# Optimization experiments

Measured on AMD Instinct MI355X. Metric: run time of the kernel, lower is better.

Reference implementation:

```python
import jax, jax.numpy as jnp
import numpy as np

HID = 1024            # hidden_dim
COND = 80             # cond_dim (mel bins)
EMB = HID // 8        # 128
D = HID // 4          # 256
NC = 2 ** 8           # num_coarse_bits = 8
NF = 2 ** 8           # num_fine_bits = 8
N, L = 32, 1024


def _vs(key, shape):
    # VarianceScaling(1.0, fan_in, truncated_normal) approximated by normal/sqrt(fan_in)
    return jax.random.normal(key, shape, jnp.float32) / jnp.sqrt(jnp.float32(shape[0]))


def setup_inputs() -> dict:
    key = jax.random.key(0)
    ks = jax.random.split(key, 16)
    x = jax.random.randint(ks[0], (N, L, 2), 0, NC, dtype=jnp.int64)
    mel = jax.random.normal(ks[1], (N, L, COND), jnp.float32)
    return {
        "x": x,
        "mel": mel,
        "R_w": _vs(ks[2], (HID, 3 * HID)),
        "R_b": jnp.zeros((3 * HID,), jnp.float32),
        "I_W": _vs(ks[3], (COND + 3 * EMB, 3 * HID)),
        "I_b": jnp.zeros((1, 3 * HID), jnp.float32),
        "O1_w": _vs(ks[4], (3 * D, 3 * D)),
        "O1_b": jnp.zeros((3 * D,), jnp.float32),
        "O2_w": _vs(ks[5], (3 * D, NC)),
        "O2_b": jnp.zeros((NC,), jnp.float32),
        "O3_w": _vs(ks[6], (D, D)),
        "O3_b": jnp.zeros((D,), jnp.float32),
        "O4_w": _vs(ks[7], (D, NF)),
        "O4_b": jnp.zeros((NF,), jnp.float32),
        "c_emb": jax.random.normal(ks[8], (NC, EMB), jnp.float32) * 0.02,
        "f_emb": jax.random.normal(ks[9], (NF, EMB), jnp.float32) * 0.02,
    }


def _mask_like(I_W):
    # zero out future-coarse embedding rows for the coarse-prediction gate halves
    m = jnp.ones_like(I_W)
    m = m.at[-EMB:, 0 * D:3 * D].set(0.0)
    m = m.at[-EMB:, 4 * D:7 * D].set(0.0)
    m = m.at[-EMB:, 8 * D:11 * D].set(0.0)
    return m


def _forward(x, mel, R_w, R_b, I_W, I_b, O1_w, O1_b, O2_w, O2_b, O3_w, O3_b, O4_w, O4_b, c_emb, f_emb):
    c = x[..., 0]
    f = x[..., 1]
    c_next = jnp.roll(c, -1, -1)
    # [N, L, COND + 3*EMB]
    inp = jnp.concatenate((mel, c_emb[c], f_emb[f], c_emb[c_next]), axis=-1)
    IW = I_W * _mask_like(I_W)
    # input projection is time-independent -> precompute for all steps: [N, L, 3H]
    xproj = jnp.einsum("nld,dh->nlh", inp, IW) + I_b[0]

    def step(h, xt):
        u1, r1, e1 = jnp.split(h @ R_w + R_b, 3, axis=-1)
        u2, r2, e2 = jnp.split(xt, 3, axis=-1)
        u = jax.nn.sigmoid(u1 + u2)
        r = jax.nn.sigmoid(r1 + r2)
        e = jnp.tanh(r * e1 + e2)
        h = u * h + (1.0 - u) * e
        return h, h

    h0 = jnp.zeros((x.shape[0], HID), xproj.dtype)
    _, hs = jax.lax.scan(step, h0, jnp.swapaxes(xproj, 0, 1))  # [L, N, H]
    hs = jnp.swapaxes(hs, 0, 1)                                 # [N, L, H]
    yc = hs[..., : 3 * D]
    yf = hs[..., 3 * D:]
    clogits = jax.nn.relu(yc @ O1_w + O1_b) @ O2_w + O2_b
    flogits = jax.nn.relu(yf @ O3_w + O3_b) @ O4_w + O4_b
    return clogits, flogits


def reference(x, mel, R_w, R_b, I_W, I_b, O1_w, O1_b, O2_w, O2_b, O3_w, O3_b, O4_w, O4_b, c_emb, f_emb):
    return _forward(x, mel, R_w, R_b, I_W, I_b, O1_w, O1_b, O2_w, O2_b,
                    O3_w, O3_b, O4_w, O4_b, c_emb, f_emb)
```

## Files before the change

kernel.cpp:

```cpp
#include <hip/hip_runtime.h>
#include <hip/hip_bf16.h>
#include <math.h>

typedef __attribute__((ext_vector_type(4))) float vf4;
typedef __attribute__((ext_vector_type(8))) short vbf8;
typedef __attribute__((ext_vector_type(8))) unsigned short vus8;

#define NWG   128
#define NTHR  256
#define LEN   1024
#define H3    3072
#define CND   80
#define EMBD  128

#define TAB1_B  0ull
#define TAB2_B  (TAB1_B + 786432ull*4)
#define TAB3_B  (TAB2_B + 786432ull*4)
#define BF_B    (TAB3_B + 786432ull*4)
#define MELA_B  (BF_B   + 4587520ull*2)
#define AF_B    (MELA_B + 3145728ull*2)
#define CNT_B   (AF_B   + 33587200ull*2)
#define W1F_B   (CNT_B + 4096ull)
#define W2F_B   (W1F_B + 1179648ull)
#define W3F_B   (W2F_B + 393216ull)
#define W4F_B   (W3F_B + 131072ull)
#define FOFS    8388608ull


__global__ __launch_bounds__(256) void make_tables(const float* __restrict__ IW,
                                                   const float* __restrict__ Ib,
                                                   const float* __restrict__ cemb,
                                                   const float* __restrict__ femb,
                                                   float* __restrict__ tab1,
                                                   float* __restrict__ tab2,
                                                   float* __restrict__ tab3) {
    int blk = blockIdx.x;
    int table = blk / 3072;
    int rem = blk % 3072;
    int row = rem / 12;
    int cc = rem % 12;
    int col = cc * 256 + threadIdx.x;
    int ofs = CND + table * EMBD;
    const float* emb = (table == 1) ? femb : cemb;
    float acc = 0.f;
    for (int k = 0; k < EMBD; ++k)
        acc += emb[row * EMBD + k] * IW[(size_t)(ofs + k) * H3 + col];
    if (table == 0) acc += Ib[col];
    if (table == 2 && ((col & 1023) < 768)) acc = 0.f;
    float* dst = (table == 0) ? tab1 : (table == 1 ? tab2 : tab3);
    dst[(size_t)row * H3 + col] = acc;
}

__global__ __launch_bounds__(256) void build_bfrag2(const float* __restrict__ Rw,
                                                    const float* __restrict__ IW,
                                                    const float* __restrict__ Rb,
                                                    unsigned short* __restrict__ Bf) {
    int idx = blockIdx.x * 256 + threadIdx.x;
    int col = idx % 3072;
    int k   = idx / 3072;
    float v;
    if (k < 1024)       v = Rw[(size_t)k * H3 + col];
    else if (k < 1104)  v = IW[(size_t)(k - 1024) * H3 + col];
    else if (k == 1104) v = Rb[col];
    else return;

    int g  = col >> 10;
    int j  = col & 1023;
    int oct = j >> 3, jo = j & 7;
    int which, c;
    if (g < 2)      { which = 0; c = g * 8 + jo; }
    else {
        which = 1;
        if (k < 1024 || k == 1104) c = jo;
        else                        c = 8 + jo;
    }
    int kk = k >> 5, r5 = k & 31;
    int lane = (r5 >> 3) * 16 + c;
    int elem = r5 & 7;
    size_t dst = (((size_t)oct * 2 + which) * 35 + kk) * 512 + lane * 8 + elem;
    __hip_bfloat16 hb = __float2bfloat16(v);
    Bf[dst] = *(unsigned short*)&hb;
}

__global__ __launch_bounds__(256) void build_melA(const float* __restrict__ mel,
                                                  unsigned short* __restrict__ MelA) {
    long idx = (long)blockIdx.x * 256 + threadIdx.x;
    int elem = idx & 7;
    int lane = (idx >> 3) & 63;
    int kkm  = (int)((idx >> 9) % 3);
    int m    = (int)((idx / 1536) & 1);
    int t    = (int)(idx / 3072);
    int b    = m * 16 + (lane & 15);
    int km   = kkm * 32 + ((lane >> 4) & 3) * 8 + elem;
    float v = (km < CND) ? mel[((size_t)b * LEN + t) * CND + km] : (km == CND ? 1.f : 0.f);
    __hip_bfloat16 hb = __float2bfloat16(v);
    MelA[idx] = *(unsigned short*)&hb;
}

__global__ __launch_bounds__(256) void build_wfrag(const float* __restrict__ W,
                                                   unsigned short* __restrict__ Wf,
                                                   int K, int N) {
    int idx = blockIdx.x * 256 + threadIdx.x;
    if (idx >= K * N) return;
    int col = idx % N;
    int k   = idx / N;
    int nt = col >> 4, c = col & 15;
    int kf = k >> 5, k5 = k & 31;
    int lane = c + 16 * (k5 >> 3);
    int elem = k5 & 7;
    size_t dst = ((size_t)nt * (K >> 5) + kf) * 512 + (size_t)lane * 8 + elem;
    __hip_bfloat16 hb = __float2bfloat16(W[idx]);
    Wf[dst] = *(unsigned short*)&hb;
}

__device__ __forceinline__ int is_sent(unsigned long long q) {
    return ((unsigned)q == 0xFFFFFFFFu) || ((unsigned)(q >> 32) == 0xFFFFFFFFu);
}

__global__ __launch_bounds__(256, 1) void scan_persist(const unsigned short* __restrict__ Bf,
                                                       const unsigned short* __restrict__ MelA,
                                                       unsigned short* __restrict__ Af,
                                                       const float* __restrict__ tab1,
                                                       const float* __restrict__ tab2,
                                                       const float* __restrict__ tab3,
                                                       const int* __restrict__ xin) {
    __shared__ float pex[4][4][256];

    int tid = threadIdx.x;
    int wg  = blockIdx.x;
    int lane = tid & 63;
    int wv = tid >> 6;
    int bh = wg >> 6;
    int jg = wg & 63;

    const unsigned short* Bp0 = Bf + (((size_t)(jg * 2 + 0) * 2 + 0) * 35) * 512 + lane * 8;
    const unsigned short* Bp1 = Bf + (((size_t)(jg * 2 + 0) * 2 + 1) * 35) * 512 + lane * 8;
    const unsigned short* Bp2 = Bf + (((size_t)(jg * 2 + 1) * 2 + 0) * 35) * 512 + lane * 8;
    const unsigned short* Bp3 = Bf + (((size_t)(jg * 2 + 1) * 2 + 1) * 35) * 512 + lane * 8;

    int bl = tid >> 4, gjl = tid & 15;
    int gb = bh * 16 + bl;
    int gj = jg * 16 + gjl;
    float hreg = 0.f;
    size_t wbase = (size_t)((bh * 32 + (gj >> 5)) * 512 +
                            (bl + 16 * ((gj >> 3) & 3)) * 8 + (gj & 7));
    int p  = gjl >> 3, jo = gjl & 7;
    int nt_ur = p * 2, nt_e = p * 2 + 1;
    int ru = ((bl >> 2) * 16 + jo) * 4 + (bl & 3);
    int rr = ((bl >> 2) * 16 + 8 + jo) * 4 + (bl & 3);

#pragma unroll 1
    for (int t = 0; t < LEN; ++t) {
        int ci = xin[(gb * LEN + t) * 2];
        int fi = xin[(gb * LEN + t) * 2 + 1];
        int cn = xin[(gb * LEN + ((t + 1) & (LEN - 1))) * 2];
        float t1u = tab1[(size_t)ci * H3 + gj];
        float t2u = tab2[(size_t)fi * H3 + gj];
        float t3u = tab3[(size_t)cn * H3 + gj];
        float t1r = tab1[(size_t)ci * H3 + 1024 + gj];
        float t2r = tab2[(size_t)fi * H3 + 1024 + gj];
        float t3r = tab3[(size_t)cn * H3 + 1024 + gj];
        float t1e = tab1[(size_t)ci * H3 + 2048 + gj];
        float t2e = tab2[(size_t)fi * H3 + 2048 + gj];
        float t3e = tab3[(size_t)cn * H3 + 2048 + gj];

        const unsigned long long* bp =
            (const unsigned long long*)(Af + (size_t)t * 32768 +
                                        (size_t)(bh * 32 + wv * 8) * 512) + lane * 2;
        unsigned long long q[16];
#pragma unroll
        for (int i = 0; i < 8; ++i) {
            q[2 * i]     = __hip_atomic_load(bp + i * 128,     __ATOMIC_RELAXED, __HIP_MEMORY_SCOPE_AGENT);
            q[2 * i + 1] = __hip_atomic_load(bp + i * 128 + 1, __ATOMIC_RELAXED, __HIP_MEMORY_SCOPE_AGENT);
        }
        for (;;) {
            int bad = 0;
#pragma unroll
            for (int i = 0; i < 16; ++i) bad |= is_sent(q[i]);
            if (!__any(bad)) break;
            __builtin_amdgcn_s_sleep(1);
#pragma unroll
            for (int i = 0; i < 8; ++i) {
                q[2 * i]     = __hip_atomic_load(bp + i * 128,     __ATOMIC_RELAXED, __HIP_MEMORY_SCOPE_AGENT);
                q[2 * i + 1] = __hip_atomic_load(bp + i * 128 + 1, __ATOMIC_RELAXED, __HIP_MEMORY_SCOPE_AGENT);
            }
        }

        vf4 acc0 = {0.f, 0.f, 0.f, 0.f}, acc1 = {0.f, 0.f, 0.f, 0.f};
        vf4 acc2 = {0.f, 0.f, 0.f, 0.f}, acc3 = {0.f, 0.f, 0.f, 0.f};
#pragma unroll
        for (int i = 0; i < 8; ++i) {
            union { unsigned long long qq[2]; vbf8 v; } ua;
            ua.qq[0] = q[2 * i]; ua.qq[1] = q[2 * i + 1];
            vbf8 a = ua.v;
            int kk = wv * 8 + i;
            acc0 = __builtin_amdgcn_mfma_f32_16x16x32_bf16(a, *(const vbf8*)(Bp0 + kk * 512), acc0, 0, 0, 0);
            acc1 = __builtin_amdgcn_mfma_f32_16x16x32_bf16(a, *(const vbf8*)(Bp1 + kk * 512), acc1, 0, 0, 0);
            acc2 = __builtin_amdgcn_mfma_f32_16x16x32_bf16(a, *(const vbf8*)(Bp2 + kk * 512), acc2, 0, 0, 0);
            acc3 = __builtin_amdgcn_mfma_f32_16x16x32_bf16(a, *(const vbf8*)(Bp3 + kk * 512), acc3, 0, 0, 0);
        }
        if (wv < 3) {
            vbf8 am = *(const vbf8*)(MelA + (size_t)t * 3072 + (size_t)(bh * 3 + wv) * 512 + lane * 8);
            acc0 = __builtin_amdgcn_mfma_f32_16x16x32_bf16(am, *(const vbf8*)(Bp0 + (32 + wv) * 512), acc0, 0, 0, 0);
            acc1 = __builtin_amdgcn_mfma_f32_16x16x32_bf16(am, *(const vbf8*)(Bp1 + (32 + wv) * 512), acc1, 0, 0, 0);
            acc2 = __builtin_amdgcn_mfma_f32_16x16x32_bf16(am, *(const vbf8*)(Bp2 + (32 + wv) * 512), acc2, 0, 0, 0);
            acc3 = __builtin_amdgcn_mfma_f32_16x16x32_bf16(am, *(const vbf8*)(Bp3 + (32 + wv) * 512), acc3, 0, 0, 0);
        }

        *(vf4*)&pex[wv][0][lane * 4] = acc0;
        *(vf4*)&pex[wv][1][lane * 4] = acc1;
        *(vf4*)&pex[wv][2][lane * 4] = acc2;
        *(vf4*)&pex[wv][3][lane * 4] = acc3;
        __syncthreads();

        float gu  = pex[0][nt_ur][ru] + pex[1][nt_ur][ru] + pex[2][nt_ur][ru] + pex[3][nt_ur][ru]
                  + t1u + t2u + t3u;
        float gr  = pex[0][nt_ur][rr] + pex[1][nt_ur][rr] + pex[2][nt_ur][rr] + pex[3][nt_ur][rr]
                  + t1r + t2r + t3r;
        float e1  = pex[0][nt_e][ru] + pex[1][nt_e][ru] + pex[2][nt_e][ru] + pex[3][nt_e][ru];
        float ge2 = pex[0][nt_e][rr] + pex[1][nt_e][rr] + pex[2][nt_e][rr] + pex[3][nt_e][rr]
                  + t1e + t2e + t3e;
        float u  = 1.f / (1.f + expf(-gu));
        float r_ = 1.f / (1.f + expf(-gr));
        float e  = tanhf(r_ * e1 + ge2);
        hreg = u * hreg + (1.f - u) * e;

        __hip_bfloat16 hb = __float2bfloat16(hreg);
        int myv = (int)(*(unsigned short*)&hb);
        int nbv = __shfl_xor(myv, 1);
        if ((tid & 1) == 0) {
            unsigned int pk = ((unsigned)myv & 0xffffu) | ((unsigned)nbv << 16);
            __hip_atomic_store((unsigned int*)(Af + (size_t)(t + 1) * 32768 + wbase), pk,
                               __ATOMIC_RELAXED, __HIP_MEMORY_SCOPE_AGENT);
        }
        __syncthreads();
    }
}

__global__ __launch_bounds__(512) void out_mlp_mfma(
        const unsigned short* __restrict__ Af,
        const unsigned short* __restrict__ W1f, const float* __restrict__ O1b,
        const unsigned short* __restrict__ W2f, const float* __restrict__ O2b,
        const unsigned short* __restrict__ W3f, const float* __restrict__ O3b,
        const unsigned short* __restrict__ W4f, const float* __restrict__ O4b,
        float* __restrict__ out) {
    __shared__ __align__(16) unsigned short Zc[2 * 24 * 512];
    __shared__ __align__(16) unsigned short Zf[2 * 8 * 512];

    int tid = threadIdx.x;
    int lane = tid & 63;
    int wv = tid >> 6;
    int m = wv >> 2;
    int q = wv & 3;
    int l = blockIdx.x;
    int c16 = lane & 15;
    int rowq = lane >> 4;

    const unsigned short* Abase = Af + (size_t)(l + 1) * 32768 +
                                  (size_t)(m * 32) * 512 + (size_t)lane * 8;

    {
        vf4 acc[12];
#pragma unroll
        for (int i = 0; i < 12; ++i) acc[i] = (vf4){0.f, 0.f, 0.f, 0.f};
        for (int kk = 0; kk < 24; ++kk) {
            vbf8 a = *(const vbf8*)(Abase + kk * 512);
#pragma unroll
            for (int i = 0; i < 12; ++i) {
                int nt = q * 12 + i;
                vbf8 b = *(const vbf8*)(W1f + ((size_t)nt * 24 + kk) * 512 + lane * 8);
                acc[i] = __builtin_amdgcn_mfma_f32_16x16x32_bf16(a, b, acc[i], 0, 0, 0);
            }
        }
#pragma unroll
        for (int i = 0; i < 12; ++i) {
            int nt = q * 12 + i;
            int col = nt * 16 + c16;
            float bias = O1b[col];
#pragma unroll
            for (int r = 0; r < 4; ++r) {
                float v = fmaxf(acc[i][r] + bias, 0.f);
                __hip_bfloat16 hb = __float2bfloat16(v);
                int my = (int)*(unsigned short*)&hb;
                int nb = __shfl_xor(my, 1);
                if ((lane & 1) == 0) {
                    unsigned pk = ((unsigned)my & 0xffffu) | ((unsigned)nb << 16);
                    int row = rowq * 4 + r;
                    int kk2 = col >> 5, k5 = col & 31;
                    int lp = row + 16 * (k5 >> 3);
                    int ep = k5 & 7;
                    *(unsigned*)&Zc[(size_t)(m * 24 + kk2) * 512 + lp * 8 + ep] = pk;
                }
            }
        }
    }
    __syncthreads();

    {
        vf4 acc[4];
#pragma unroll
        for (int i = 0; i < 4; ++i) acc[i] = (vf4){0.f, 0.f, 0.f, 0.f};
        for (int kk = 0; kk < 24; ++kk) {
            vbf8 a = *(const vbf8*)(Zc + (size_t)(m * 24 + kk) * 512 + lane * 8);
#pragma unroll
            for (int i = 0; i < 4; ++i) {
                int nt = q * 4 + i;
                vbf8 b = *(const vbf8*)(W2f + ((size_t)nt * 24 + kk) * 512 + lane * 8);
                acc[i] = __builtin_amdgcn_mfma_f32_16x16x32_bf16(a, b, acc[i], 0, 0, 0);
            }
        }
#pragma unroll
        for (int i = 0; i < 4; ++i) {
            int nt = q * 4 + i;
            int col = nt * 16 + c16;
            float bias = O2b[col];
#pragma unroll
            for (int r = 0; r < 4; ++r) {
                int nn = m * 16 + rowq * 4 + r;
                out[((size_t)nn * 1024 + l) * 256 + col] = acc[i][r] + bias;
            }
        }
    }

    {
        vf4 acc[4];
#pragma unroll
        for (int i = 0; i < 4; ++i) acc[i] = (vf4){0.f, 0.f, 0.f, 0.f};
        for (int kf = 0; kf < 8; ++kf) {
            vbf8 a = *(const vbf8*)(Abase + (24 + kf) * 512);
#pragma unroll
            for (int i = 0; i < 4; ++i) {
                int nt = q * 4 + i;
                vbf8 b = *(const vbf8*)(W3f + ((size_t)nt * 8 + kf) * 512 + lane * 8);
                acc[i] = __builtin_amdgcn_mfma_f32_16x16x32_bf16(a, b, acc[i], 0, 0, 0);
            }
        }
#pragma unroll
        for (int i = 0; i < 4; ++i) {
            int nt = q * 4 + i;
            int col = nt * 16 + c16;
            float bias = O3b[col];
#pragma unroll
            for (int r = 0; r < 4; ++r) {
                float v = fmaxf(acc[i][r] + bias, 0.f);
                __hip_bfloat16 hb = __float2bfloat16(v);
                int my = (int)*(unsigned short*)&hb;
                int nb = __shfl_xor(my, 1);
                if ((lane & 1) == 0) {
                    unsigned pk = ((unsigned)my & 0xffffu) | ((unsigned)nb << 16);
                    int row = rowq * 4 + r;
                    int kk2 = col >> 5, k5 = col & 31;
                    int lp = row + 16 * (k5 >> 3);
                    int ep = k5 & 7;
                    *(unsigned*)&Zf[(size_t)(m * 8 + kk2) * 512 + lp * 8 + ep] = pk;
                }
            }
        }
    }
    __syncthreads();

    {
        vf4 acc[4];
#pragma unroll
        for (int i = 0; i < 4; ++i) acc[i] = (vf4){0.f, 0.f, 0.f, 0.f};
        for (int kf = 0; kf < 8; ++kf) {
            vbf8 a = *(const vbf8*)(Zf + (size_t)(m * 8 + kf) * 512 + lane * 8);
#pragma unroll
            for (int i = 0; i < 4; ++i) {
                int nt = q * 4 + i;
                vbf8 b = *(const vbf8*)(W4f + ((size_t)nt * 8 + kf) * 512 + lane * 8);
                acc[i] = __builtin_amdgcn_mfma_f32_16x16x32_bf16(a, b, acc[i], 0, 0, 0);
            }
        }
#pragma unroll
        for (int i = 0; i < 4; ++i) {
            int nt = q * 4 + i;
            int col = nt * 16 + c16;
            float bias = O4b[col];
#pragma unroll
            for (int r = 0; r < 4; ++r) {
                int nn = m * 16 + rowq * 4 + r;
                out[FOFS + ((size_t)nn * 1024 + l) * 256 + col] = acc[i][r] + bias;
            }
        }
    }
}

extern "C" void kernel_launch(void* const* d_in, const int* in_sizes, int n_in,
                              void* d_out, int out_size, void* d_ws, size_t ws_size,
                              hipStream_t stream) {
    const int*   x    = (const int*)d_in[0];
    const float* mel  = (const float*)d_in[1];
    const float* Rw   = (const float*)d_in[2];
    const float* Rb   = (const float*)d_in[3];
    const float* IW   = (const float*)d_in[4];
    const float* Ib   = (const float*)d_in[5];
    const float* O1w  = (const float*)d_in[6];
    const float* O1b  = (const float*)d_in[7];
    const float* O2w  = (const float*)d_in[8];
    const float* O2b  = (const float*)d_in[9];
    const float* O3w  = (const float*)d_in[10];
    const float* O3b  = (const float*)d_in[11];
    const float* O4w  = (const float*)d_in[12];
    const float* O4b  = (const float*)d_in[13];
    const float* cemb = (const float*)d_in[14];
    const float* femb = (const float*)d_in[15];
    char* wsb = (char*)d_ws;
    float* out = (float*)d_out;

    float* tab1 = (float*)(wsb + TAB1_B);
    float* tab2 = (float*)(wsb + TAB2_B);
    float* tab3 = (float*)(wsb + TAB3_B);
    unsigned short* Bf   = (unsigned short*)(wsb + BF_B);
    unsigned short* MelA = (unsigned short*)(wsb + MELA_B);
    unsigned short* Af   = (unsigned short*)(wsb + AF_B);
    unsigned short* W1f  = (unsigned short*)(wsb + W1F_B);
    unsigned short* W2f  = (unsigned short*)(wsb + W2F_B);
    unsigned short* W3f  = (unsigned short*)(wsb + W3F_B);
    unsigned short* W4f  = (unsigned short*)(wsb + W4F_B);

    make_tables<<<9216, 256, 0, stream>>>(IW, Ib, cemb, femb, tab1, tab2, tab3);
    hipMemsetAsync((void*)Bf, 0, 4587520ull * 2, stream);
    build_bfrag2<<<13440, 256, 0, stream>>>(Rw, IW, Rb, Bf);
    build_melA<<<12288, 256, 0, stream>>>(mel, MelA);
    build_wfrag<<<2304, 256, 0, stream>>>(O1w, W1f, 768, 768);
    build_wfrag<<<768,  256, 0, stream>>>(O2w, W2f, 768, 256);
    build_wfrag<<<256,  256, 0, stream>>>(O3w, W3f, 256, 256);
    build_wfrag<<<256,  256, 0, stream>>>(O4w, W4f, 256, 256);
    hipMemsetAsync((void*)Af, 0xFF, 33587200ull * 2, stream);
    hipMemsetAsync((void*)Af, 0, 65536, stream);

    scan_persist<<<NWG, NTHR, 0, stream>>>(Bf, MelA, Af, tab1, tab2, tab3, x);

    out_mlp_mfma<<<1024, 512, 0, stream>>>(Af, W1f, O1b, W2f, O2b, W3f, O3b, W4f, O4b, out);
}
```

Before: 2.702 ms.

## Halve scan workgroups, doubling columns per workgroup with 8 waves

New measurement: 3.378 ms. 1.25x slower.

```diff
diff --git a/kernel.cpp b/kernel.cpp
--- a/kernel.cpp
+++ b/kernel.cpp
@@ -6,8 +6,8 @@
 typedef __attribute__((ext_vector_type(8))) short vbf8;
 typedef __attribute__((ext_vector_type(8))) unsigned short vus8;
 
-#define NWG   128
-#define NTHR  256
+#define NWG   64
+#define NTHR  512
 #define LEN   1024
 #define H3    3072
 #define CND   80
@@ -117,30 +117,34 @@
     return ((unsigned)q == 0xFFFFFFFFu) || ((unsigned)(q >> 32) == 0xFFFFFFFFu);
 }
 
-__global__ __launch_bounds__(256, 1) void scan_persist(const unsigned short* __restrict__ Bf,
+__global__ __launch_bounds__(512, 1) void scan_persist(const unsigned short* __restrict__ Bf,
                                                        const unsigned short* __restrict__ MelA,
                                                        unsigned short* __restrict__ Af,
                                                        const float* __restrict__ tab1,
                                                        const float* __restrict__ tab2,
                                                        const float* __restrict__ tab3,
                                                        const int* __restrict__ xin) {
-    __shared__ float pex[4][4][256];
+    __shared__ float pex[8][8][256];
 
     int tid = threadIdx.x;
     int wg  = blockIdx.x;
     int lane = tid & 63;
     int wv = tid >> 6;
-    int bh = wg >> 6;
-    int jg = wg & 63;
-
-    const unsigned short* Bp0 = Bf + (((size_t)(jg * 2 + 0) * 2 + 0) * 35) * 512 + lane * 8;
-    const unsigned short* Bp1 = Bf + (((size_t)(jg * 2 + 0) * 2 + 1) * 35) * 512 + lane * 8;
-    const unsigned short* Bp2 = Bf + (((size_t)(jg * 2 + 1) * 2 + 0) * 35) * 512 + lane * 8;
-    const unsigned short* Bp3 = Bf + (((size_t)(jg * 2 + 1) * 2 + 1) * 35) * 512 + lane * 8;
-
-    int bl = tid >> 4, gjl = tid & 15;
+    int bh = wg >> 5;
+    int jg = wg & 31;
+
+    const unsigned short* Bp0 = Bf + (((size_t)(jg * 4 + 0) * 2 + 0) * 35) * 512 + lane * 8;
+    const unsigned short* Bp1 = Bf + (((size_t)(jg * 4 + 0) * 2 + 1) * 35) * 512 + lane * 8;
+    const unsigned short* Bp2 = Bf + (((size_t)(jg * 4 + 1) * 2 + 0) * 35) * 512 + lane * 8;
+    const unsigned short* Bp3 = Bf + (((size_t)(jg * 4 + 1) * 2 + 1) * 35) * 512 + lane * 8;
+    const unsigned short* Bp4 = Bf + (((size_t)(jg * 4 + 2) * 2 + 0) * 35) * 512 + lane * 8;
+    const unsigned short* Bp5 = Bf + (((size_t)(jg * 4 + 2) * 2 + 1) * 35) * 512 + lane * 8;
+    const unsigned short* Bp6 = Bf + (((size_t)(jg * 4 + 3) * 2 + 0) * 35) * 512 + lane * 8;
+    const unsigned short* Bp7 = Bf + (((size_t)(jg * 4 + 3) * 2 + 1) * 35) * 512 + lane * 8;
+
+    int bl = tid >> 5, gjl = tid & 31;
     int gb = bh * 16 + bl;
-    int gj = jg * 16 + gjl;
+    int gj = jg * 32 + gjl;
     float hreg = 0.f;
     size_t wbase = (size_t)((bh * 32 + (gj >> 5)) * 512 +
                             (bl + 16 * ((gj >> 3) & 3)) * 8 + (gj & 7));
@@ -166,21 +170,21 @@
 
         const unsigned long long* bp =
             (const unsigned long long*)(Af + (size_t)t * 32768 +
-                                        (size_t)(bh * 32 + wv * 8) * 512) + lane * 2;
-        unsigned long long q[16];
-#pragma unroll
-        for (int i = 0; i < 8; ++i) {
+                                        (size_t)(bh * 32 + wv * 4) * 512) + lane * 2;
+        unsigned long long q[8];
+#pragma unroll
+        for (int i = 0; i < 4; ++i) {
             q[2 * i]     = __hip_atomic_load(bp + i * 128,     __ATOMIC_RELAXED, __HIP_MEMORY_SCOPE_AGENT);
             q[2 * i + 1] = __hip_atomic_load(bp + i * 128 + 1, __ATOMIC_RELAXED, __HIP_MEMORY_SCOPE_AGENT);
         }
         for (;;) {
             int bad = 0;
 #pragma unroll
-            for (int i = 0; i < 16; ++i) bad |= is_sent(q[i]);
+            for (int i = 0; i < 8; ++i) bad |= is_sent(q[i]);
             if (!__any(bad)) break;
             __builtin_amdgcn_s_sleep(1);
 #pragma unroll
-            for (int i = 0; i < 8; ++i) {
+            for (int i = 0; i < 4; ++i) {
                 q[2 * i]     = __hip_atomic_load(bp + i * 128,     __ATOMIC_RELAXED, __HIP_MEMORY_SCOPE_AGENT);
                 q[2 * i + 1] = __hip_atomic_load(bp + i * 128 + 1, __ATOMIC_RELAXED, __HIP_MEMORY_SCOPE_AGENT);
             }
@@ -188,37 +192,59 @@
 
         vf4 acc0 = {0.f, 0.f, 0.f, 0.f}, acc1 = {0.f, 0.f, 0.f, 0.f};
         vf4 acc2 = {0.f, 0.f, 0.f, 0.f}, acc3 = {0.f, 0.f, 0.f, 0.f};
-#pragma unroll
-        for (int i = 0; i < 8; ++i) {
+        vf4 acc4 = {0.f, 0.f, 0.f, 0.f}, acc5 = {0.f, 0.f, 0.f, 0.f};
+        vf4 acc6 = {0.f, 0.f, 0.f, 0.f}, acc7 = {0.f, 0.f, 0.f, 0.f};
+#pragma unroll
+        for (int i = 0; i < 4; ++i) {
             union { unsigned long long qq[2]; vbf8 v; } ua;
             ua.qq[0] = q[2 * i]; ua.qq[1] = q[2 * i + 1];
             vbf8 a = ua.v;
-            int kk = wv * 8 + i;
+            int kk = wv * 4 + i;
             acc0 = __builtin_amdgcn_mfma_f32_16x16x32_bf16(a, *(const vbf8*)(Bp0 + kk * 512), acc0, 0, 0, 0);
             acc1 = __builtin_amdgcn_mfma_f32_16x16x32_bf16(a, *(const vbf8*)(Bp1 + kk * 512), acc1, 0, 0, 0);
             acc2 = __builtin_amdgcn_mfma_f32_16x16x32_bf16(a, *(const vbf8*)(Bp2 + kk * 512), acc2, 0, 0, 0);
             acc3 = __builtin_amdgcn_mfma_f32_16x16x32_bf16(a, *(const vbf8*)(Bp3 + kk * 512), acc3, 0, 0, 0);
-        }
-        if (wv < 3) {
-            vbf8 am = *(const vbf8*)(MelA + (size_t)t * 3072 + (size_t)(bh * 3 + wv) * 512 + lane * 8);
-            acc0 = __builtin_amdgcn_mfma_f32_16x16x32_bf16(am, *(const vbf8*)(Bp0 + (32 + wv) * 512), acc0, 0, 0, 0);
-            acc1 = __builtin_amdgcn_mfma_f32_16x16x32_bf16(am, *(const vbf8*)(Bp1 + (32 + wv) * 512), acc1, 0, 0, 0);
-            acc2 = __builtin_amdgcn_mfma_f32_16x16x32_bf16(am, *(const vbf8*)(Bp2 + (32 + wv) * 512), acc2, 0, 0, 0);
-            acc3 = __builtin_amdgcn_mfma_f32_16x16x32_bf16(am, *(const vbf8*)(Bp3 + (32 + wv) * 512), acc3, 0, 0, 0);
+            acc4 = __builtin_amdgcn_mfma_f32_16x16x32_bf16(a, *(const vbf8*)(Bp4 + kk * 512), acc4, 0, 0, 0);
+            acc5 = __builtin_amdgcn_mfma_f32_16x16x32_bf16(a, *(const vbf8*)(Bp5 + kk * 512), acc5, 0, 0, 0);
+            acc6 = __builtin_amdgcn_mfma_f32_16x16x32_bf16(a, *(const vbf8*)(Bp6 + kk * 512), acc6, 0, 0, 0);
+            acc7 = __builtin_amdgcn_mfma_f32_16x16x32_bf16(a, *(const vbf8*)(Bp7 + kk * 512), acc7, 0, 0, 0);
+        }
+        if (wv < 6) {
+            int kq = wv >> 1;
+            vbf8 am = *(const vbf8*)(MelA + (size_t)t * 3072 + (size_t)(bh * 3 + kq) * 512 + lane * 8);
+            if ((wv & 1) == 0) {
+                acc0 = __builtin_amdgcn_mfma_f32_16x16x32_bf16(am, *(const vbf8*)(Bp0 + (32 + kq) * 512), acc0, 0, 0, 0);
+                acc1 = __builtin_amdgcn_mfma_f32_16x16x32_bf16(am, *(const vbf8*)(Bp1 + (32 + kq) * 512), acc1, 0, 0, 0);
+                acc2 = __builtin_amdgcn_mfma_f32_16x16x32_bf16(am, *(const vbf8*)(Bp2 + (32 + kq) * 512), acc2, 0, 0, 0);
+                acc3 = __builtin_amdgcn_mfma_f32_16x16x32_bf16(am, *(const vbf8*)(Bp3 + (32 + kq) * 512), acc3, 0, 0, 0);
+            } else {
+                acc4 = __builtin_amdgcn_mfma_f32_16x16x32_bf16(am, *(const vbf8*)(Bp4 + (32 + kq) * 512), acc4, 0, 0, 0);
+                acc5 = __builtin_amdgcn_mfma_f32_16x16x32_bf16(am, *(const vbf8*)(Bp5 + (32 + kq) * 512), acc5, 0, 0, 0);
+                acc6 = __builtin_amdgcn_mfma_f32_16x16x32_bf16(am, *(const vbf8*)(Bp6 + (32 + kq) * 512), acc6, 0, 0, 0);
+                acc7 = __builtin_amdgcn_mfma_f32_16x16x32_bf16(am, *(const vbf8*)(Bp7 + (32 + kq) * 512), acc7, 0, 0, 0);
+            }
         }
 
         *(vf4*)&pex[wv][0][lane * 4] = acc0;
         *(vf4*)&pex[wv][1][lane * 4] = acc1;
         *(vf4*)&pex[wv][2][lane * 4] = acc2;
         *(vf4*)&pex[wv][3][lane * 4] = acc3;
+        *(vf4*)&pex[wv][4][lane * 4] = acc4;
+        *(vf4*)&pex[wv][5][lane * 4] = acc5;
+        *(vf4*)&pex[wv][6][lane * 4] = acc6;
+        *(vf4*)&pex[wv][7][lane * 4] = acc7;
         __syncthreads();
 
-        float gu  = pex[0][nt_ur][ru] + pex[1][nt_ur][ru] + pex[2][nt_ur][ru] + pex[3][nt_ur][ru]
+        float gu  = ((pex[0][nt_ur][ru] + pex[1][nt_ur][ru]) + (pex[2][nt_ur][ru] + pex[3][nt_ur][ru]))
+                  + ((pex[4][nt_ur][ru] + pex[5][nt_ur][ru]) + (pex[6][nt_ur][ru] + pex[7][nt_ur][ru]))
                   + t1u + t2u + t3u;
-        float gr  = pex[0][nt_ur][rr] + pex[1][nt_ur][rr] + pex[2][nt_ur][rr] + pex[3][nt_ur][rr]
+        float gr  = ((pex[0][nt_ur][rr] + pex[1][nt_ur][rr]) + (pex[2][nt_ur][rr] + pex[3][nt_ur][rr]))
+                  + ((pex[4][nt_ur][rr] + pex[5][nt_ur][rr]) + (pex[6][nt_ur][rr] + pex[7][nt_ur][rr]))
                   + t1r + t2r + t3r;
-        float e1  = pex[0][nt_e][ru] + pex[1][nt_e][ru] + pex[2][nt_e][ru] + pex[3][nt_e][ru];
-        float ge2 = pex[0][nt_e][rr] + pex[1][nt_e][rr] + pex[2][nt_e][rr] + pex[3][nt_e][rr]
+        float e1  = ((pex[0][nt_e][ru] + pex[1][nt_e][ru]) + (pex[2][nt_e][ru] + pex[3][nt_e][ru]))
+                  + ((pex[4][nt_e][ru] + pex[5][nt_e][ru]) + (pex[6][nt_e][ru] + pex[7][nt_e][ru]));
+        float ge2 = ((pex[0][nt_e][rr] + pex[1][nt_e][rr]) + (pex[2][nt_e][rr] + pex[3][nt_e][rr]))
+                  + ((pex[4][nt_e][rr] + pex[5][nt_e][rr]) + (pex[6][nt_e][rr] + pex[7][nt_e][rr]))
                   + t1e + t2e + t3e;
         float u  = 1.f / (1.f + expf(-gu));
         float r_ = 1.f / (1.f + expf(-gr));
```
